# Kernel tuning notes

Measured on AMD Instinct MI355X. Metric: run time of the kernel, lower is better.

The kernel has to match this reference:

```python
import jax, jax.numpy as jnp
import numpy as np

N_NODES = 50000


def _gcn_conv(x, W, b, src, dst, n_nodes):
    """PyG GCNConv: add self-loops, symmetric deg^-1/2 norm, linear, aggregate, bias."""
    # add self-loops
    loop = jnp.arange(n_nodes, dtype=src.dtype)
    s = jnp.concatenate([src, loop])  # [E+N]
    d = jnp.concatenate([dst, loop])  # [E+N]
    # degree of A + I computed over targets
    deg = jax.ops.segment_sum(jnp.ones_like(d, dtype=x.dtype), d, num_segments=n_nodes)
    dinv = jnp.where(deg > 0, jax.lax.rsqrt(deg), 0.0)
    norm = dinv[s] * dinv[d]  # [E+N]
    h = x @ W  # [N, out] transform-first (in_dim >= out_dim friendly)
    msg = h[s] * norm[:, None]  # [E+N, out]
    out = jax.ops.segment_sum(msg, d, num_segments=n_nodes)
    return out + b


def setup_inputs() -> dict:
    key = jax.random.key(0)
    k1, k2, k3, k4 = jax.random.split(key, 4)
    in_dim, hidden, out_dim = 256, 128, 64
    E = 800000
    x = jax.random.normal(k1, (N_NODES, in_dim), dtype=jnp.float32)
    edge_index = jax.random.randint(k2, (2, E), 0, N_NODES, dtype=jnp.int64)
    W1 = jax.random.normal(k3, (in_dim, hidden), dtype=jnp.float32) / np.sqrt(in_dim)
    b1 = jnp.zeros((hidden,), dtype=jnp.float32)
    W2 = jax.random.normal(k4, (hidden, out_dim), dtype=jnp.float32) / np.sqrt(hidden)
    b2 = jnp.zeros((out_dim,), dtype=jnp.float32)
    return {"x": x, "edge_index": edge_index, "W1": W1, "b1": b1, "W2": W2, "b2": b2}


def reference(x, edge_index, W1, b1, W2, b2):
    src, dst = edge_index[0], edge_index[1]
    h = _gcn_conv(x, W1, b1, src, dst, N_NODES)
    h = jax.nn.relu(h)
    out = _gcn_conv(h, W2, b2, src, dst, N_NODES)
    return out
```

## Files before the change

kernel.cpp:

```cpp
#include <hip/hip_runtime.h>

#define N_NODES 50000
#define NCH 256
#define NBKT 256

typedef short bf16x8 __attribute__((ext_vector_type(8)));
typedef float f32x4 __attribute__((ext_vector_type(4)));

__device__ inline unsigned short f2bf(float f) {
    union { float f; unsigned u; } v; v.f = f;
    unsigned u = v.u;
    unsigned lsb = (u >> 16) & 1u;
    u += 0x7fffu + lsb;
    return (unsigned short)(u >> 16);
}

__device__ inline float bf2f(unsigned short h) {
    union { unsigned u; float f; } v; v.u = ((unsigned)h) << 16;
    return v.f;
}

__global__ __launch_bounds__(256) void prep(const int* __restrict__ dst,
                                            int* __restrict__ cnt, int E, int epc,
                                            const float* __restrict__ W1,
                                            const float* __restrict__ W2,
                                            unsigned short* __restrict__ B1h,
                                            unsigned short* __restrict__ B1l,
                                            unsigned short* __restrict__ B2h,
                                            unsigned short* __restrict__ B2l) {
    const int c = blockIdx.x;
    if (c < NCH) {
        __shared__ int h[NBKT];
        h[threadIdx.x] = 0;
        __syncthreads();
        const int e0 = c * epc;
        const int e1 = min(E, e0 + epc);
        for (int e = e0 + threadIdx.x; e < e1; e += 256)
            atomicAdd(&h[dst[e] >> 8], 1);
        __syncthreads();
        cnt[c * NBKT + threadIdx.x] = h[threadIdx.x];
        return;
    }
    int i = (c - NCH) * 256 + threadIdx.x;
    const float* W;
    unsigned short *Th, *Tl;
    int K, logM, idx;
    if (i < 32768) { W = W1; Th = B1h; Tl = B1l; K = 256; logM = 7; idx = i; }
    else if (i < 32768 + 8192) { W = W2; Th = B2h; Tl = B2l; K = 128; logM = 6; idx = i - 32768; }
    else return;
    const int M = 1 << logM;
    const int KS = K / 32;
    int k = idx >> logM;
    int n = idx & (M - 1);
    float v = W[idx];
    unsigned short h = f2bf(v);
    unsigned short l = f2bf(v - bf2f(h));
    int g = n >> 4, n16 = n & 15, ks = k >> 5, quad = (k >> 3) & 3, j = k & 7;
    size_t o = ((size_t)((g * KS + ks) * 64 + quad * 16 + n16)) * 8 + j;
    Th[o] = h;
    Tl[o] = l;
}

__global__ __launch_bounds__(256) void bkt_scan_chunks(const int* __restrict__ cnt,
                                                       int* __restrict__ off,
                                                       int* __restrict__ total) {
    __shared__ int sh[256];
    const int b = blockIdx.x;
    const int t = threadIdx.x;
    int v = cnt[t * NBKT + b];
    sh[t] = v;
    __syncthreads();
    for (int o = 1; o < 256; o <<= 1) {
        int u = (t >= o) ? sh[t - o] : 0;
        __syncthreads();
        sh[t] += u;
        __syncthreads();
    }
    off[t * NBKT + b] = sh[t] - v;
    if (t == 255) total[b] = sh[255];
}

__global__ __launch_bounds__(256) void bkt_scatter(const int* __restrict__ src,
                                                   const int* __restrict__ dst,
                                                   const int* __restrict__ off,
                                                   const int* __restrict__ total,
                                                   unsigned* __restrict__ pairs,
                                                   int E, int epc) {
    __shared__ int sh[256];
    __shared__ int cur[NBKT];
    const int c = blockIdx.x;
    const int t = threadIdx.x;
    int v = total[t];
    sh[t] = v;
    __syncthreads();
    for (int o = 1; o < 256; o <<= 1) {
        int u = (t >= o) ? sh[t - o] : 0;
        __syncthreads();
        sh[t] += u;
        __syncthreads();
    }
    cur[t] = (sh[t] - v) + off[c * NBKT + t];
    __syncthreads();
    const int e0 = c * epc;
    const int e1 = min(E, e0 + epc);
    for (int e = e0 + t; e < e1; e += 256) {
        int s = src[e];
        int d = dst[e];
        int pos = atomicAdd(&cur[d >> 8], 1);
        pairs[pos] = ((unsigned)s << 8) | (unsigned)(d & 255);
    }
}

__global__ __launch_bounds__(256) void bkt_csr(const unsigned* __restrict__ pairs,
                                               const int* __restrict__ total,
                                               int* __restrict__ rowptr,
                                               int* __restrict__ csr_src,
                                               float* __restrict__ dinv, int N) {
    __shared__ int lh[256];
    __shared__ int sc[256];
    __shared__ int lcur[256];
    const int b = blockIdx.x;
    const int t = threadIdx.x;

    sc[t] = total[t];
    __syncthreads();
    for (int o = 1; o < 256; o <<= 1) {
        int u = (t >= o) ? sc[t - o] : 0;
        __syncthreads();
        sc[t] += u;
        __syncthreads();
    }
    const int eend = sc[b];
    const int ebase = eend - total[b];
    const int node0 = b << 8;

    lh[t] = 0;
    __syncthreads();
    for (int e = ebase + t; e < eend; e += 256)
        atomicAdd(&lh[pairs[e] & 255u], 1);
    __syncthreads();
    int v = lh[t];
    sc[t] = v;
    __syncthreads();
    for (int o = 1; o < 256; o <<= 1) {
        int u = (t >= o) ? sc[t - o] : 0;
        __syncthreads();
        sc[t] += u;
        __syncthreads();
    }
    const int excl = sc[t] - v;
    lcur[t] = ebase + excl;
    const int node = node0 + t;
    if (node <= N) {
        rowptr[node] = ebase + excl;
        if (node < N) dinv[node] = rsqrtf((float)(v + 1));
    }
    __syncthreads();
    for (int e = ebase + t; e < eend; e += 256) {
        unsigned p = pairs[e];
        int pos = atomicAdd(&lcur[p & 255u], 1);
        csr_src[pos] = (int)(p >> 8);
    }
}

template <int K, int M>
__global__ __launch_bounds__(M * 4) void gemm_mfma_v4(const float* __restrict__ A,
                                                      const unsigned short* __restrict__ Bfh,
                                                      const unsigned short* __restrict__ Bfl,
                                                      const float* __restrict__ dinv,
                                                      unsigned short* __restrict__ Cb, int N) {
    const int KS = K / 32;
    const int THREADS = M * 4;
    const int CPT = 512 / THREADS;
    const int PL = 64 * 40;
    const int CPAIRS = M / 32;

    __shared__ __align__(16) unsigned short Ah[2 * PL];
    __shared__ __align__(16) unsigned short Al[2 * PL];

    const int tid = threadIdx.x;
    const int wave = tid >> 6;
    const int lane = tid & 63;
    const int n16 = lane & 15;
    const int quad = lane >> 4;
    const int cpair = wave & (CPAIRS - 1);
    const int rpair = wave / CPAIRS;
    const int row0 = blockIdx.x * 64;

    bf16x8 bh[2][2], bl[2][2];
    auto loadB = [&](int ks, int par) {
#pragma unroll
        for (int ct = 0; ct < 2; ct++) {
            const int g = cpair * 2 + ct;
            const size_t o = ((size_t)(g * KS + ks) * 64 + lane) * 8;
            bh[par][ct] = *(const bf16x8*)(Bfh + o);
            bl[par][ct] = *(const bf16x8*)(Bfl + o);
        }
    };
    loadB(0, 0);

    int srow[CPT], sc4[CPT];
    const float* aptr[CPT];
#pragma unroll
    for (int p = 0; p < CPT; p++) {
        int q = p * THREADS + tid;
        srow[p] = q >> 3;
        sc4[p] = q & 7;
        int grow = row0 + srow[p];
        if (grow >= N) grow = N - 1;
        aptr[p] = A + (size_t)grow * K + sc4[p] * 4;
    }

    float4 pre[CPT];
#pragma unroll
    for (int p = 0; p < CPT; p++) pre[p] = *(const float4*)(aptr[p]);

#pragma unroll
    for (int p = 0; p < CPT; p++) {
        ushort4 h4, l4;
        unsigned short* hp = (unsigned short*)&h4;
        unsigned short* lp = (unsigned short*)&l4;
        float av[4] = {pre[p].x, pre[p].y, pre[p].z, pre[p].w};
#pragma unroll
        for (int j = 0; j < 4; j++) {
            unsigned short h = f2bf(av[j]);
            hp[j] = h;
            lp[j] = f2bf(av[j] - bf2f(h));
        }
        *(ushort4*)(Ah + srow[p] * 40 + sc4[p] * 4) = h4;
        *(ushort4*)(Al + srow[p] * 40 + sc4[p] * 4) = l4;
    }
    if (KS > 1) {
#pragma unroll
        for (int p = 0; p < CPT; p++) pre[p] = *(const float4*)(aptr[p] + 32);
    }
    __syncthreads();

    f32x4 acc[2][2] = {};

#pragma unroll
    for (int ks = 0; ks < KS; ks++) {
        const int cur = ks & 1;
        if (ks + 1 < KS) loadB(ks + 1, cur ^ 1);
#pragma unroll
        for (int rt = 0; rt < 2; rt++) {
            const int ro = cur * PL + (rpair * 32 + rt * 16 + n16) * 40 + quad * 8;
            bf16x8 ah = *(const bf16x8*)(Ah + ro);
            bf16x8 al = *(const bf16x8*)(Al + ro);
#pragma unroll
            for (int ct = 0; ct < 2; ct++) {
                acc[rt][ct] = __builtin_amdgcn_mfma_f32_16x16x32_bf16(ah, bh[cur][ct], acc[rt][ct], 0, 0, 0);
                acc[rt][ct] = __builtin_amdgcn_mfma_f32_16x16x32_bf16(ah, bl[cur][ct], acc[rt][ct], 0, 0, 0);
                acc[rt][ct] = __builtin_amdgcn_mfma_f32_16x16x32_bf16(al, bh[cur][ct], acc[rt][ct], 0, 0, 0);
            }
        }
        if (ks + 1 < KS) {
            const int nxt = (cur ^ 1) * PL;
#pragma unroll
            for (int p = 0; p < CPT; p++) {
                ushort4 h4, l4;
                unsigned short* hp = (unsigned short*)&h4;
                unsigned short* lp = (unsigned short*)&l4;
                float av[4] = {pre[p].x, pre[p].y, pre[p].z, pre[p].w};
#pragma unroll
                for (int j = 0; j < 4; j++) {
                    unsigned short h = f2bf(av[j]);
                    hp[j] = h;
                    lp[j] = f2bf(av[j] - bf2f(h));
                }
                *(ushort4*)(Ah + nxt + srow[p] * 40 + sc4[p] * 4) = h4;
                *(ushort4*)(Al + nxt + srow[p] * 40 + sc4[p] * 4) = l4;
            }
            if (ks + 2 < KS) {
#pragma unroll
                for (int p = 0; p < CPT; p++)
                    pre[p] = *(const float4*)(aptr[p] + (ks + 2) * 32);
            }
        }
        __syncthreads();
    }

#pragma unroll
    for (int rt = 0; rt < 2; rt++) {
#pragma unroll
        for (int ct = 0; ct < 2; ct++) {
            const int col = cpair * 32 + ct * 16 + n16;
            const int rbase = row0 + rpair * 32 + rt * 16 + quad * 4;
#pragma unroll
            for (int r = 0; r < 4; r++) {
                int orow = rbase + r;
                if (orow < N) {
                    Cb[(size_t)orow * M + col] = f2bf(dinv[orow] * acc[rt][ct][r]);
                }
            }
        }
    }
}

template <int K, int M>
__global__ __launch_bounds__(256) void gather_gemm2(const unsigned short* __restrict__ hnb,
                                                    const int* __restrict__ rowptr,
                                                    const int* __restrict__ csr_src,
                                                    const float* __restrict__ dinv,
                                                    const float* __restrict__ bias,
                                                    const unsigned short* __restrict__ Bfh,
                                                    const unsigned short* __restrict__ Bfl,
                                                    unsigned short* __restrict__ Cb, int N) {
    const int KS = K / 32;
    const int CPAIRS = M / 32;
    const int PLP = 64 * 40;

    __shared__ __align__(16) unsigned short Ah[KS * PLP];

    const int tid = threadIdx.x;
    const int wave = tid >> 6;
    const int lane = tid & 63;
    const int n16 = lane & 15;
    const int quad = lane >> 4;
    const int cpair = wave & (CPAIRS - 1);
    const int rpair = wave / CPAIRS;
    const int row0 = blockIdx.x * 64;

    bf16x8 bh[2][2], bl[2][2];
    auto loadB = [&](int ks, int par) {
#pragma unroll
        for (int ct = 0; ct < 2; ct++) {
            const int g = cpair * 2 + ct;
            const size_t o = ((size_t)(g * KS + ks) * 64 + lane) * 8;
            bh[par][ct] = *(const bf16x8*)(Bfh + o);
            bl[par][ct] = *(const bf16x8*)(Bfl + o);
        }
    };
    loadB(0, 0);

    {
        const int j = tid & 15;
        const int nl = tid >> 4;
        const int panel = j >> 2;
        const int coff = (j & 3) * 8;
#pragma unroll
        for (int p = 0; p < 4; p++) {
            const int r = p * 16 + nl;
            const int g = row0 + r;
            unsigned short* ldst = Ah + panel * PLP + r * 40 + coff;
            if (g < N) {
                float acc[8];
                {
                    bf16x8 v = *(const bf16x8*)(hnb + (size_t)g * K + j * 8);
#pragma unroll
                    for (int i = 0; i < 8; i++) acc[i] = bf2f((unsigned short)v[i]);
                }
                int e = rowptr[g];
                const int end = rowptr[g + 1];
                for (; e + 3 < end; e += 4) {
                    int s0 = csr_src[e];
                    int s1 = csr_src[e + 1];
                    int s2 = csr_src[e + 2];
                    int s3 = csr_src[e + 3];
                    bf16x8 v0 = *(const bf16x8*)(hnb + (size_t)s0 * K + j * 8);
                    bf16x8 v1 = *(const bf16x8*)(hnb + (size_t)s1 * K + j * 8);
                    bf16x8 v2 = *(const bf16x8*)(hnb + (size_t)s2 * K + j * 8);
                    bf16x8 v3 = *(const bf16x8*)(hnb + (size_t)s3 * K + j * 8);
#pragma unroll
                    for (int i = 0; i < 8; i++) {
                        acc[i] += (bf2f((unsigned short)v0[i]) + bf2f((unsigned short)v1[i])) +
                                  (bf2f((unsigned short)v2[i]) + bf2f((unsigned short)v3[i]));
                    }
                }
                for (; e < end; e++) {
                    int s0 = csr_src[e];
                    bf16x8 v0 = *(const bf16x8*)(hnb + (size_t)s0 * K + j * 8);
#pragma unroll
                    for (int i = 0; i < 8; i++) acc[i] += bf2f((unsigned short)v0[i]);
                }
                const float s = dinv[g];
                bf16x8 rr;
#pragma unroll
                for (int i = 0; i < 8; i++)
                    rr[i] = (short)f2bf(fmaxf(s * acc[i] + bias[j * 8 + i], 0.0f));
                *(bf16x8*)ldst = rr;
            } else {
                bf16x8 z = {};
                *(bf16x8*)ldst = z;
            }
        }
    }
    __syncthreads();

    f32x4 acc[2][2] = {};
#pragma unroll
    for (int ks = 0; ks < KS; ks++) {
        const int cur = ks & 1;
        if (ks + 1 < KS) loadB(ks + 1, cur ^ 1);
#pragma unroll
        for (int rt = 0; rt < 2; rt++) {
            const int ro = ks * PLP + (rpair * 32 + rt * 16 + n16) * 40 + quad * 8;
            bf16x8 ah = *(const bf16x8*)(Ah + ro);
#pragma unroll
            for (int ct = 0; ct < 2; ct++) {
                acc[rt][ct] = __builtin_amdgcn_mfma_f32_16x16x32_bf16(ah, bh[cur][ct], acc[rt][ct], 0, 0, 0);
                acc[rt][ct] = __builtin_amdgcn_mfma_f32_16x16x32_bf16(ah, bl[cur][ct], acc[rt][ct], 0, 0, 0);
            }
        }
    }

#pragma unroll
    for (int rt = 0; rt < 2; rt++) {
#pragma unroll
        for (int ct = 0; ct < 2; ct++) {
            const int col = cpair * 32 + ct * 16 + n16;
            const int rbase = row0 + rpair * 32 + rt * 16 + quad * 4;
#pragma unroll
            for (int r = 0; r < 4; r++) {
                int orow = rbase + r;
                if (orow < N) {
                    Cb[(size_t)orow * M + col] = f2bf(dinv[orow] * acc[rt][ct][r]);
                }
            }
        }
    }
}

template <int M>
__global__ __launch_bounds__(256) void gather_to_f32(const unsigned short* __restrict__ hnb,
                                                     const int* __restrict__ rowptr,
                                                     const int* __restrict__ csr_src,
                                                     const float* __restrict__ dinv,
                                                     const float* __restrict__ bias,
                                                     float* __restrict__ outp, int n) {
    const int MQ = M / 8;
    const int GPB = 256 / MQ;
    int g = blockIdx.x * GPB + threadIdx.x / MQ;
    int j = threadIdx.x % MQ;
    if (g >= n) return;

    float acc[8];
    {
        bf16x8 v = *(const bf16x8*)(hnb + (size_t)g * M + j * 8);
#pragma unroll
        for (int i = 0; i < 8; i++) acc[i] = bf2f((unsigned short)v[i]);
    }

    int e = rowptr[g];
    const int end = rowptr[g + 1];
    for (; e + 3 < end; e += 4) {
        int s0 = csr_src[e];
        int s1 = csr_src[e + 1];
        int s2 = csr_src[e + 2];
        int s3 = csr_src[e + 3];
        bf16x8 v0 = *(const bf16x8*)(hnb + (size_t)s0 * M + j * 8);
        bf16x8 v1 = *(const bf16x8*)(hnb + (size_t)s1 * M + j * 8);
        bf16x8 v2 = *(const bf16x8*)(hnb + (size_t)s2 * M + j * 8);
        bf16x8 v3 = *(const bf16x8*)(hnb + (size_t)s3 * M + j * 8);
#pragma unroll
        for (int i = 0; i < 8; i++) {
            acc[i] += (bf2f((unsigned short)v0[i]) + bf2f((unsigned short)v1[i])) +
                      (bf2f((unsigned short)v2[i]) + bf2f((unsigned short)v3[i]));
        }
    }
    for (; e < end; e++) {
        int s0 = csr_src[e];
        bf16x8 v0 = *(const bf16x8*)(hnb + (size_t)s0 * M + j * 8);
#pragma unroll
        for (int i = 0; i < 8; i++) acc[i] += bf2f((unsigned short)v0[i]);
    }

    const float s = dinv[g];
    float r[8];
#pragma unroll
    for (int i = 0; i < 8; i++) r[i] = s * acc[i] + bias[j * 8 + i];
    float* op = outp + (size_t)g * M + j * 8;
    *(float4*)(op) = make_float4(r[0], r[1], r[2], r[3]);
    *(float4*)(op + 4) = make_float4(r[4], r[5], r[6], r[7]);
}

extern "C" void kernel_launch(void* const* d_in, const int* in_sizes, int n_in,
                              void* d_out, int out_size, void* d_ws, size_t ws_size,
                              hipStream_t stream) {
    const float* x  = (const float*)d_in[0];
    const int*   ei = (const int*)d_in[1];
    const float* W1 = (const float*)d_in[2];
    const float* b1 = (const float*)d_in[3];
    const float* W2 = (const float*)d_in[4];
    const float* b2 = (const float*)d_in[5];

    const int N = N_NODES;
    const int E = in_sizes[1] / 2;
    const int* src = ei;
    const int* dst = ei + E;

    char* ws = (char*)d_ws;
    size_t off = 0;
    auto carve = [&](size_t bytes) {
        char* p = ws + off;
        off += (bytes + 255) & ~(size_t)255;
        return p;
    };
    int*      cnt     = (int*)     carve((size_t)NCH * NBKT * 4);
    int*      offm    = (int*)     carve((size_t)NCH * NBKT * 4);
    int*      total   = (int*)     carve((size_t)NBKT * 4);
    unsigned* pairs   = (unsigned*)carve((size_t)E * 4);
    int*      rowptr  = (int*)     carve((size_t)(N + 1) * 4);
    int*      csr_src = (int*)     carve((size_t)E * 4);
    float*    dinv    = (float*)   carve((size_t)N * 4);
    unsigned short* W1th = (unsigned short*)carve((size_t)256 * 128 * 2);
    unsigned short* W1tl = (unsigned short*)carve((size_t)256 * 128 * 2);
    unsigned short* W2th = (unsigned short*)carve((size_t)128 * 64 * 2);
    unsigned short* W2tl = (unsigned short*)carve((size_t)128 * 64 * 2);
    unsigned short* hn1b = (unsigned short*)carve((size_t)N * 128 * 2);
    unsigned short* hn2b = (unsigned short*)carve((size_t)N * 64 * 2);

    const int epc = (E + NCH - 1) / NCH;
    const int nbk = (N + 255) >> 8;

    prep<<<NCH + 160, 256, 0, stream>>>(dst, cnt, E, epc, W1, W2, W1th, W1tl, W2th, W2tl);
    bkt_scan_chunks<<<NBKT, 256, 0, stream>>>(cnt, offm, total);
    bkt_scatter<<<NCH, 256, 0, stream>>>(src, dst, offm, total, pairs, E, epc);
    bkt_csr<<<nbk, 256, 0, stream>>>(pairs, total, rowptr, csr_src, dinv, N);

    const int GB = (N + 63) / 64;

    gemm_mfma_v4<256, 128><<<GB, 512, 0, stream>>>(x, W1th, W1tl, dinv, hn1b, N);

    gather_gemm2<128, 64><<<GB, 256, 0, stream>>>(hn1b, rowptr, csr_src, dinv, b1,
                                                  W2th, W2tl, hn2b, N);

    {
        const int GPB = 256 / (64 / 8);
        gather_to_f32<64><<<(N + GPB - 1) / GPB, 256, 0, stream>>>(
            hn2b, rowptr, csr_src, dinv, b2, (float*)d_out, N);
    }
}
```

Baseline: 198.5 us.

## Split gathers into column-plane kernels and unfuse layer-2 gather from GEMM

```diff
diff --git a/kernel.cpp b/kernel.cpp
--- a/kernel.cpp
+++ b/kernel.cpp
@@ -290,27 +290,81 @@
             for (int r = 0; r < 4; r++) {
                 int orow = rbase + r;
                 if (orow < N) {
-                    Cb[(size_t)orow * M + col] = f2bf(dinv[orow] * acc[rt][ct][r]);
+                    unsigned short ob = f2bf(dinv[orow] * acc[rt][ct][r]);
+                    Cb[(size_t)(col >> 5) * ((size_t)N_NODES * 32) +
+                       (size_t)orow * 32 + (col & 31)] = ob;
                 }
             }
         }
     }
 }
 
+__global__ __launch_bounds__(256) void gather1_xcd(const unsigned short* __restrict__ hnb,
+                                                   const int* __restrict__ rowptr,
+                                                   const int* __restrict__ csr_src,
+                                                   const float* __restrict__ dinv,
+                                                   const float* __restrict__ bias,
+                                                   unsigned short* __restrict__ outp,
+                                                   int N) {
+    const size_t PL = (size_t)N_NODES * 32;
+    const int q = blockIdx.x & 3;
+    const int tile = blockIdx.x >> 2;
+    const int j = threadIdx.x & 3;
+    const int r = threadIdx.x >> 2;
+    const int g = tile * 64 + r;
+    if (g >= N) return;
+
+    const unsigned short* plane = hnb + (size_t)q * PL + j * 8;
+    float acc[8];
+    {
+        bf16x8 v = *(const bf16x8*)(plane + (size_t)g * 32);
+#pragma unroll
+        for (int i = 0; i < 8; i++) acc[i] = bf2f((unsigned short)v[i]);
+    }
+    int e = rowptr[g];
+    const int end = rowptr[g + 1];
+    for (; e + 3 < end; e += 4) {
+        int s0 = csr_src[e];
+        int s1 = csr_src[e + 1];
+        int s2 = csr_src[e + 2];
+        int s3 = csr_src[e + 3];
+        bf16x8 v0 = *(const bf16x8*)(plane + (size_t)s0 * 32);
+        bf16x8 v1 = *(const bf16x8*)(plane + (size_t)s1 * 32);
+        bf16x8 v2 = *(const bf16x8*)(plane + (size_t)s2 * 32);
+        bf16x8 v3 = *(const bf16x8*)(plane + (size_t)s3 * 32);
+#pragma unroll
+        for (int i = 0; i < 8; i++) {
+            acc[i] += (bf2f((unsigned short)v0[i]) + bf2f((unsigned short)v1[i])) +
+                      (bf2f((unsigned short)v2[i]) + bf2f((unsigned short)v3[i]));
+        }
+    }
+    for (; e < end; e++) {
+        int s0 = csr_src[e];
+        bf16x8 v0 = *(const bf16x8*)(plane + (size_t)s0 * 32);
+#pragma unroll
+        for (int i = 0; i < 8; i++) acc[i] += bf2f((unsigned short)v0[i]);
+    }
+
+    const float s = dinv[g];
+    bf16x8 rr;
+#pragma unroll
+    for (int i = 0; i < 8; i++)
+        rr[i] = (short)f2bf(fmaxf(s * acc[i] + bias[q * 32 + j * 8 + i], 0.0f));
+    *(bf16x8*)(outp + (size_t)q * PL + (size_t)g * 32 + j * 8) = rr;
+}
+
 template <int K, int M>
-__global__ __launch_bounds__(256) void gather_gemm2(const unsigned short* __restrict__ hnb,
-                                                    const int* __restrict__ rowptr,
-                                                    const int* __restrict__ csr_src,
-                                                    const float* __restrict__ dinv,
-                                                    const float* __restrict__ bias,
-                                                    const unsigned short* __restrict__ Bfh,
-                                                    const unsigned short* __restrict__ Bfl,
-                                                    unsigned short* __restrict__ Cb, int N) {
+__global__ __launch_bounds__(M * 4) void gemm_mfma_bfA(const unsigned short* __restrict__ A,
+                                                       const unsigned short* __restrict__ Bfh,
+                                                       const unsigned short* __restrict__ Bfl,
+                                                       const float* __restrict__ dinv,
+                                                       unsigned short* __restrict__ Cb, int N) {
     const int KS = K / 32;
+    const int PL = 64 * 40;
     const int CPAIRS = M / 32;
-    const int PLP = 64 * 40;
-
-    __shared__ __align__(16) unsigned short Ah[KS * PLP];
+    const size_t APL = (size_t)N_NODES * 32;
+
+    __shared__ __align__(16) unsigned short Ah[2 * PL];
 
     const int tid = threadIdx.x;
     const int wave = tid >> 6;
@@ -333,68 +387,39 @@
     };
     loadB(0, 0);
 
+    const int srow = tid >> 2;
+    const int sc8 = tid & 3;
+    const unsigned short* aptr;
     {
-        const int j = tid & 15;
-        const int nl = tid >> 4;
-        const int panel = j >> 2;
-        const int coff = (j & 3) * 8;
-#pragma unroll
-        for (int p = 0; p < 4; p++) {
-            const int r = p * 16 + nl;
-            const int g = row0 + r;
-            unsigned short* ldst = Ah + panel * PLP + r * 40 + coff;
-            if (g < N) {
-                float acc[8];
-                {
-                    bf16x8 v = *(const bf16x8*)(hnb + (size_t)g * K + j * 8);
-#pragma unroll
-                    for (int i = 0; i < 8; i++) acc[i] = bf2f((unsigned short)v[i]);
-                }
-                int e = rowptr[g];
-                const int end = rowptr[g + 1];
-                for (; e + 3 < end; e += 4) {
-                    int s0 = csr_src[e];
-                    int s1 = csr_src[e + 1];
-                    int s2 = csr_src[e + 2];
-                    int s3 = csr_src[e + 3];
-                    bf16x8 v0 = *(const bf16x8*)(hnb + (size_t)s0 * K + j * 8);
-                    bf16x8 v1 = *(const bf16x8*)(hnb + (size_t)s1 * K + j * 8);
-                    bf16x8 v2 = *(const bf16x8*)(hnb + (size_t)s2 * K + j * 8);
-                    bf16x8 v3 = *(const bf16x8*)(hnb + (size_t)s3 * K + j * 8);
-#pragma unroll
-                    for (int i = 0; i < 8; i++) {
-                        acc[i] += (bf2f((unsigned short)v0[i]) + bf2f((unsigned short)v1[i])) +
-                                  (bf2f((unsigned short)v2[i]) + bf2f((unsigned short)v3[i]));
-                    }
-                }
-                for (; e < end; e++) {
-                    int s0 = csr_src[e];
-                    bf16x8 v0 = *(const bf16x8*)(hnb + (size_t)s0 * K + j * 8);
-#pragma unroll
-                    for (int i = 0; i < 8; i++) acc[i] += bf2f((unsigned short)v0[i]);
-                }
-                const float s = dinv[g];
-                bf16x8 rr;
-#pragma unroll
-                for (int i = 0; i < 8; i++)
-                    rr[i] = (short)f2bf(fmaxf(s * acc[i] + bias[j * 8 + i], 0.0f));
-                *(bf16x8*)ldst = rr;
-            } else {
-                bf16x8 z = {};
-                *(bf16x8*)ldst = z;
-            }
-        }
-    }
+        int grow = row0 + srow;
+        if (grow >= N) grow = N - 1;
+        aptr = A + (size_t)grow * 32 + sc8 * 8;
+    }
+
+    bf16x8 pre = *(const bf16x8*)(aptr);
+
+    {
+        ushort4* d0 = (ushort4*)(Ah + srow * 40 + sc8 * 8);
+        ushort4 lo, hi;
+        unsigned short* lp = (unsigned short*)&lo;
+        unsigned short* hp = (unsigned short*)&hi;
+#pragma unroll
+        for (int j = 0; j < 4; j++) { lp[j] = (unsigned short)pre[j]; hp[j] = (unsigned short)pre[j + 4]; }
+        d0[0] = lo;
+        d0[1] = hi;
+    }
+    if (KS > 1) pre = *(const bf16x8*)(aptr + APL);
     __syncthreads();
 
     f32x4 acc[2][2] = {};
+
 #pragma unroll
     for (int ks = 0; ks < KS; ks++) {
         const int cur = ks & 1;
         if (ks + 1 < KS) loadB(ks + 1, cur ^ 1);
 #pragma unroll
         for (int rt = 0; rt < 2; rt++) {
-            const int ro = ks * PLP + (rpair * 32 + rt * 16 + n16) * 40 + quad * 8;
+            const int ro = cur * PL + (rpair * 32 + rt * 16 + n16) * 40 + quad * 8;
             bf16x8 ah = *(const bf16x8*)(Ah + ro);
 #pragma unroll
             for (int ct = 0; ct < 2; ct++) {
@@ -402,6 +427,19 @@
                 acc[rt][ct] = __builtin_amdgcn_mfma_f32_16x16x32_bf16(ah, bl[cur][ct], acc[rt][ct], 0, 0, 0);
             }
         }
+        if (ks + 1 < KS) {
+            const int nxt = (cur ^ 1) * PL;
+            ushort4* d0 = (ushort4*)(Ah + nxt + srow * 40 + sc8 * 8);
+            ushort4 lo, hi;
+            unsigned short* lp = (unsigned short*)&lo;
+            unsigned short* hp = (unsigned short*)&hi;
+#pragma unroll
+            for (int j = 0; j < 4; j++) { lp[j] = (unsigned short)pre[j]; hp[j] = (unsigned short)pre[j + 4]; }
+            d0[0] = lo;
+            d0[1] = hi;
+            if (ks + 2 < KS) pre = *(const bf16x8*)(aptr + (size_t)(ks + 2) * APL);
+        }
+        __syncthreads();
     }
 
 #pragma unroll
@@ -421,26 +459,26 @@
     }
 }
 
-template <int M>
-__global__ __launch_bounds__(256) void gather_to_f32(const unsigned short* __restrict__ hnb,
-                                                     const int* __restrict__ rowptr,
-                                                     const int* __restrict__ csr_src,
-                                                     const float* __restrict__ dinv,
-                                                     const float* __restrict__ bias,
-                                                     float* __restrict__ outp, int n) {
-    const int MQ = M / 8;
-    const int GPB = 256 / MQ;
-    int g = blockIdx.x * GPB + threadIdx.x / MQ;
-    int j = threadIdx.x % MQ;
-    if (g >= n) return;
-
+__global__ __launch_bounds__(256) void gather_f32_xcd(const unsigned short* __restrict__ hnb,
+                                                      const int* __restrict__ rowptr,
+                                                      const int* __restrict__ csr_src,
+                                                      const float* __restrict__ dinv,
+                                                      const float* __restrict__ bias,
+                                                      float* __restrict__ outp, int N) {
+    const int h = blockIdx.x & 1;
+    const int tile = blockIdx.x >> 1;
+    const int j = threadIdx.x & 3;
+    const int r = threadIdx.x >> 2;
+    const int g = tile * 64 + r;
+    if (g >= N) return;
+
+    const unsigned short* base = hnb + h * 32 + j * 8;
     float acc[8];
     {
-        bf16x8 v = *(const bf16x8*)(hnb + (size_t)g * M + j * 8);
+        bf16x8 v = *(const bf16x8*)(base + (size_t)g * 64);
 #pragma unroll
         for (int i = 0; i < 8; i++) acc[i] = bf2f((unsigned short)v[i]);
     }
-
     int e = rowptr[g];
     const int end = rowptr[g + 1];
     for (; e + 3 < end; e += 4) {
@@ -448,10 +486,10 @@
         int s1 = csr_src[e + 1];
         int s2 = csr_src[e + 2];
         int s3 = csr_src[e + 3];
-        bf16x8 v0 = *(const bf16x8*)(hnb + (size_t)s0 * M + j * 8);
-        bf16x8 v1 = *(const bf16x8*)(hnb + (size_t)s1 * M + j * 8);
-        bf16x8 v2 = *(const bf16x8*)(hnb + (size_t)s2 * M + j * 8);
-        bf16x8 v3 = *(const bf16x8*)(hnb + (size_t)s3 * M + j * 8);
+        bf16x8 v0 = *(const bf16x8*)(base + (size_t)s0 * 64);
+        bf16x8 v1 = *(const bf16x8*)(base + (size_t)s1 * 64);
+        bf16x8 v2 = *(const bf16x8*)(base + (size_t)s2 * 64);
+        bf16x8 v3 = *(const bf16x8*)(base + (size_t)s3 * 64);
 #pragma unroll
         for (int i = 0; i < 8; i++) {
             acc[i] += (bf2f((unsigned short)v0[i]) + bf2f((unsigned short)v1[i])) +
@@ -460,18 +498,18 @@
     }
     for (; e < end; e++) {
         int s0 = csr_src[e];
-        bf16x8 v0 = *(const bf16x8*)(hnb + (size_t)s0 * M + j * 8);
+        bf16x8 v0 = *(const bf16x8*)(base + (size_t)s0 * 64);
 #pragma unroll
         for (int i = 0; i < 8; i++) acc[i] += bf2f((unsigned short)v0[i]);
     }
 
     const float s = dinv[g];
-    float r[8];
-#pragma unroll
-    for (int i = 0; i < 8; i++) r[i] = s * acc[i] + bias[j * 8 + i];
-    float* op = outp + (size_t)g * M + j * 8;
-    *(float4*)(op) = make_float4(r[0], r[1], r[2], r[3]);
-    *(float4*)(op + 4) = make_float4(r[4], r[5], r[6], r[7]);
+    float rr[8];
+#pragma unroll
+    for (int i = 0; i < 8; i++) rr[i] = s * acc[i] + bias[h * 32 + j * 8 + i];
+    float* op = outp + (size_t)g * 64 + h * 32 + j * 8;
+    *(float4*)(op) = make_float4(rr[0], rr[1], rr[2], rr[3]);
+    *(float4*)(op + 4) = make_float4(rr[4], rr[5], rr[6], rr[7]);
 }
 
 extern "C" void kernel_launch(void* const* d_in, const int* in_sizes, int n_in,
@@ -507,27 +545,25 @@
     unsigned short* W1tl = (unsigned short*)carve((size_t)256 * 128 * 2);
     unsigned short* W2th = (unsigned short*)carve((size_t)128 * 64 * 2);
     unsigned short* W2tl = (unsigned short*)carve((size_t)128 * 64 * 2);
-    unsigned short* hn1b = (unsigned short*)carve((size_t)N * 128 * 2);
+    unsigned short* hn1q = (unsigned short*)carve((size_t)N * 128 * 2);
+    unsigned short* h1q  = (unsigned short*)carve((size_t)N * 128 * 2);
     unsigned short* hn2b = (unsigned short*)carve((size_t)N * 64 * 2);
 
     const int epc = (E + NCH - 1) / NCH;
     const int nbk = (N + 255) >> 8;
+    const int GB = (N + 63) / 64;
 
     prep<<<NCH + 160, 256, 0, stream>>>(dst, cnt, E, epc, W1, W2, W1th, W1tl, W2th, W2tl);
     bkt_scan_chunks<<<NBKT, 256, 0, stream>>>(cnt, offm, total);
     bkt_scatter<<<NCH, 256, 0, stream>>>(src, dst, offm, total, pairs, E, epc);
     bkt_csr<<<nbk, 256, 0, stream>>>(pairs, total, rowptr, csr_src, dinv, N);
 
-    const int GB = (N + 63) / 64;
-
-    gemm_mfma_v4<256, 128><<<GB, 512, 0, stream>>>(x, W1th, W1tl, dinv, hn1b, N);
-
-    gather_gemm2<128, 64><<<GB, 256, 0, stream>>>(hn1b, rowptr, csr_src, dinv, b1,
-                                                  W2th, W2tl, hn2b, N);
-
-    {
-        const int GPB = 256 / (64 / 8);
-        gather_to_f32<64><<<(N + GPB - 1) / GPB, 256, 0, stream>>>(
-            hn2b, rowptr, csr_src, dinv, b2, (float*)d_out, N);
-    }
-}
+    gemm_mfma_v4<256, 128><<<GB, 512, 0, stream>>>(x, W1th, W1tl, dinv, hn1q, N);
+
+    gather1_xcd<<<4 * GB, 256, 0, stream>>>(hn1q, rowptr, csr_src, dinv, b1, h1q, N);
+
+    gemm_mfma_bfA<128, 64><<<GB, 256, 0, stream>>>(h1q, W2th, W2tl, dinv, hn2b, N);
+
+    gather_f32_xcd<<<2 * GB, 256, 0, stream>>>(hn2b, rowptr, csr_src, dinv, b2,
+                                               (float*)d_out, N);
+}
```

New measurement: 207.4 us. 4.4% more time.
